# Kernel tuning notes

Measured on AMD Instinct MI355X. Metric: run time of the kernel, lower is better.

The kernel has to match this reference:

```python
import jax, jax.numpy as jnp
import numpy as np

N, M, D, H, T = 8192, 8192, 64, 32, 8
KERNEL_SCALE = 1.0


def setup_inputs() -> dict:
    key = jax.random.key(0)
    ks = jax.random.split(key, 8)
    s1 = 1.0 / np.sqrt(D)
    s2 = 1.0 / np.sqrt(H)
    return {
        "X": jax.random.normal(ks[0], (N, D), jnp.float32),
        "Y": jax.random.normal(ks[1], (M, D), jnp.float32),
        "Y_target": jax.random.normal(ks[2], (M, T), jnp.float32),
        "W1": jax.random.normal(ks[3], (D, H), jnp.float32) * s1,
        "b1": jnp.zeros((H,), jnp.float32),
        "W2": jax.random.normal(ks[4], (H, H), jnp.float32) * s2,
        "b2": jnp.zeros((H,), jnp.float32),
        "W3": jax.random.normal(ks[5], (H, H), jnp.float32) * s2,
        "b3": jnp.zeros((H,), jnp.float32),
    }


def _mlp(x, W1, b1, W2, b2, W3, b3):
    h = jax.nn.relu(x @ W1 + b1)
    h = jax.nn.relu(h @ W2 + b2)
    return jax.nn.relu(h @ W3 + b3)


def reference(X, Y, Y_target, W1, b1, W2, b2, W3, b3):
    Xf = _mlp(X, W1, b1, W2, b2, W3, b3)  # [N, H]
    Yf = _mlp(Y, W1, b1, W2, b2, W3, b3)  # [M, H]
    sq = (
        jnp.sum(Xf * Xf, axis=1, keepdims=True)
        + jnp.sum(Yf * Yf, axis=1)[None, :]
        - 2.0 * (Xf @ Yf.T)
    )
    sq = jnp.maximum(sq, 0.0)  # guard tiny negatives from cancellation
    kernel = jnp.exp(-sq / (2.0 * KERNEL_SCALE**2))  # [N, M]
    weights = kernel / jnp.sum(kernel, axis=1, keepdims=True)
    return weights @ Y_target  # [N, T]
```

## Files before the change

kernel.cpp:

```cpp
#include <hip/hip_runtime.h>
#include <hip/hip_bf16.h>
#include <cstddef>

#define N_ROWS 8192
#define M_ROWS 8192
#define D_IN   64
#define H_DIM  32
#define T_OUT  8
#define FDIM   48

#define NSPLIT   32
#define JSLICE   (M_ROWS / NSPLIT)
#define JTILE    32
#define NTILES   (JSLICE / JTILE)
#define LOG2E    1.4426950408889634f
#define NHALF_SC (-0.72134752044448169f)

typedef _Float16 half8  __attribute__((ext_vector_type(8)));
typedef _Float16 half4v __attribute__((ext_vector_type(4)));
typedef __fp16   fp16x2 __attribute__((ext_vector_type(2)));
typedef float    f32x16 __attribute__((ext_vector_type(16)));

__device__ __forceinline__ half8 ld_h8(const _Float16* p) {
    return *(const half8*)p;
}

__global__ __launch_bounds__(256) void feat_kernel(
    const float* __restrict__ X, const float* __restrict__ Y,
    const float* __restrict__ W1, const float* __restrict__ b1,
    const float* __restrict__ W2, const float* __restrict__ b2,
    const float* __restrict__ W3, const float* __restrict__ b3,
    _Float16* __restrict__ fh, _Float16* __restrict__ fl)
{
    __shared__ float xs [32 * 65];
    __shared__ float w1l[64 * 36];
    __shared__ float w2l[32 * 36];
    __shared__ float w3l[32 * 36];
    __shared__ float h1t[32 * 33];
    __shared__ float h2t[32 * 33];
    __shared__ float psums[8 * 32];
    __shared__ float bl[96];

    const int tid = threadIdx.x;
    const int rowbase = blockIdx.x * 32;
    const bool isX = rowbase < N_ROWS;
    const float* src = isX ? (X + (size_t)rowbase * D_IN)
                           : (Y + (size_t)(rowbase - N_ROWS) * D_IN);

    {
        const float4* g4 = (const float4*)src;
        int i0 = tid * 2;
        float4 v0 = g4[i0], v1 = g4[i0 + 1];
        int f0 = tid * 8;
        int r = f0 >> 6, c = f0 & 63;
        float* dst = xs + r * 65 + c;
        dst[0] = v0.x; dst[1] = v0.y; dst[2] = v0.z; dst[3] = v0.w;
        dst[4] = v1.x; dst[5] = v1.y; dst[6] = v1.z; dst[7] = v1.w;
    }
    {
        const float4* g4 = (const float4*)W1;
        int i0 = tid * 2;
        float4 v0 = g4[i0], v1 = g4[i0 + 1];
        int f0 = tid * 8;
        int r = f0 >> 5, c = f0 & 31;
        float* dst = w1l + r * 36 + c;
        ((float4*)dst)[0] = v0; ((float4*)dst)[1] = v1;
    }
    {
        int f0 = tid * 4;
        int r = f0 >> 5, c = f0 & 31;
        *(float4*)(w2l + r * 36 + c) = ((const float4*)W2)[tid];
        *(float4*)(w3l + r * 36 + c) = ((const float4*)W3)[tid];
    }
    if (tid < 32) { bl[tid] = b1[tid]; bl[32 + tid] = b2[tid]; bl[64 + tid] = b3[tid]; }
    __syncthreads();

    const int r  = tid & 31;
    const int c0 = (tid >> 5) * 4;

    float4 a1 = *(const float4*)(bl + c0);
    #pragma unroll
    for (int k = 0; k < 64; ++k) {
        float xv = xs[r * 65 + k];
        float4 w = *(const float4*)(w1l + k * 36 + c0);
        a1.x = fmaf(xv, w.x, a1.x);
        a1.y = fmaf(xv, w.y, a1.y);
        a1.z = fmaf(xv, w.z, a1.z);
        a1.w = fmaf(xv, w.w, a1.w);
    }
    h1t[(c0 + 0) * 33 + r] = fmaxf(a1.x, 0.f);
    h1t[(c0 + 1) * 33 + r] = fmaxf(a1.y, 0.f);
    h1t[(c0 + 2) * 33 + r] = fmaxf(a1.z, 0.f);
    h1t[(c0 + 3) * 33 + r] = fmaxf(a1.w, 0.f);
    __syncthreads();

    float4 a2 = *(const float4*)(bl + 32 + c0);
    #pragma unroll
    for (int k = 0; k < 32; ++k) {
        float xv = h1t[k * 33 + r];
        float4 w = *(const float4*)(w2l + k * 36 + c0);
        a2.x = fmaf(xv, w.x, a2.x);
        a2.y = fmaf(xv, w.y, a2.y);
        a2.z = fmaf(xv, w.z, a2.z);
        a2.w = fmaf(xv, w.w, a2.w);
    }
    h2t[(c0 + 0) * 33 + r] = fmaxf(a2.x, 0.f);
    h2t[(c0 + 1) * 33 + r] = fmaxf(a2.y, 0.f);
    h2t[(c0 + 2) * 33 + r] = fmaxf(a2.z, 0.f);
    h2t[(c0 + 3) * 33 + r] = fmaxf(a2.w, 0.f);
    __syncthreads();

    float4 a3 = *(const float4*)(bl + 64 + c0);
    #pragma unroll
    for (int k = 0; k < 32; ++k) {
        float xv = h2t[k * 33 + r];
        float4 w = *(const float4*)(w3l + k * 36 + c0);
        a3.x = fmaf(xv, w.x, a3.x);
        a3.y = fmaf(xv, w.y, a3.y);
        a3.z = fmaf(xv, w.z, a3.z);
        a3.w = fmaf(xv, w.w, a3.w);
    }
    float v0 = fmaxf(a3.x, 0.f), v1 = fmaxf(a3.y, 0.f);
    float v2 = fmaxf(a3.z, 0.f), v3 = fmaxf(a3.w, 0.f);

    psums[(tid >> 5) * 32 + r] = v0 * v0 + v1 * v1 + v2 * v2 + v3 * v3;

    const float scale = isX ? LOG2E : 1.0f;
    union { _Float16 h[4]; uint2 u; } hh, ll;
    float sv0 = v0 * scale, sv1 = v1 * scale, sv2 = v2 * scale, sv3 = v3 * scale;
    hh.h[0] = (_Float16)sv0; hh.h[1] = (_Float16)sv1;
    hh.h[2] = (_Float16)sv2; hh.h[3] = (_Float16)sv3;
    ll.h[0] = (_Float16)(sv0 - (float)hh.h[0]);
    ll.h[1] = (_Float16)(sv1 - (float)hh.h[1]);
    ll.h[2] = (_Float16)(sv2 - (float)hh.h[2]);
    ll.h[3] = (_Float16)(sv3 - (float)hh.h[3]);
    const size_t fo = (size_t)(rowbase + r) * FDIM + c0;
    *(uint2*)(fh + fo) = hh.u;
    *(uint2*)(fl + fo) = ll.u;

    __syncthreads();
    if (tid < 32) {
        float nrm = 0.f;
        #pragma unroll
        for (int g = 0; g < 8; ++g) nrm += psums[g * 32 + tid];
        float qn = NHALF_SC * nrm;
        float d32 = isX ? qn : 1.0f;
        float d33 = isX ? 1.0f : qn;
        union { _Float16 h[16]; uint4 q[2]; } eh, el;
        #pragma unroll
        for (int i = 0; i < 16; ++i) { eh.h[i] = (_Float16)0.f; el.h[i] = (_Float16)0.f; }
        _Float16 h32 = (_Float16)d32, h33 = (_Float16)d33;
        eh.h[0] = h32; eh.h[1] = h33;
        el.h[0] = (_Float16)(d32 - (float)h32);
        el.h[1] = (_Float16)(d33 - (float)h33);
        const size_t eo = (size_t)(rowbase + tid) * FDIM + 32;
        *(uint4*)(fh + eo) = eh.q[0]; *(uint4*)(fh + eo + 8) = eh.q[1];
        *(uint4*)(fl + eo) = el.q[0]; *(uint4*)(fl + eo + 8) = el.q[1];
    }
}

__global__ __launch_bounds__(256) void ytt_kernel(
    const float* __restrict__ Yt,
    _Float16* __restrict__ yfh, _Float16* __restrict__ yfl)
{
    const int idx = blockIdx.x * 256 + threadIdx.x;
    const int lane = idx & 63;
    const int jtg  = idx >> 6;
    const int g    = jtg & 3;
    const int jt   = jtg >> 2;
    const int t    = lane & 31;
    const int h    = lane >> 5;
    const int j    = jt * 32 + g * 8 + h * 4;
    union { _Float16 hh[4]; uint2 u; } H, L;
    #pragma unroll
    for (int i = 0; i < 4; ++i) {
        float v = (t < T_OUT) ? Yt[(size_t)(j + i) * T_OUT + t]
                              : (t == 8 ? 1.0f : 0.0f);
        _Float16 hi = (_Float16)v;
        H.hh[i] = hi;
        L.hh[i] = (_Float16)(v - (float)hi);
    }
    *(uint2*)(yfh + (size_t)idx * 4) = H.u;
    *(uint2*)(yfl + (size_t)idx * 4) = L.u;
}

__global__ __launch_bounds__(256, 4) void pair_kernel(
    const _Float16* __restrict__ fh, const _Float16* __restrict__ fl,
    const _Float16* __restrict__ yfh, const _Float16* __restrict__ yfl,
    float* __restrict__ pout, float* __restrict__ psum)
{
    const int tid  = threadIdx.x;
    const int wave = tid >> 6;
    const int lane = tid & 63;
    const int n    = lane & 31;
    const int h    = lane >> 5;

    const int rowbase = blockIdx.x * 128 + wave * 32;
    const int s       = blockIdx.y;
    const int jstart  = s * JSLICE;

    const _Float16* qb  = fh + (size_t)(rowbase + n) * FDIM + h * 8;
    const _Float16* qbl = fl + (size_t)(rowbase + n) * FDIM + h * 8;
    half8 qh0 = ld_h8(qb);        half8 qh1 = ld_h8(qb + 16);
    half8 qh2 = ld_h8(qb + 32);
    half8 ql0 = ld_h8(qbl);       half8 ql1 = ld_h8(qbl + 16);
    half8 ql2 = ld_h8(qbl + 32);

    f32x16 o = {};

    for (int jt = 0; jt < NTILES; ++jt) {
        const int jbase = jstart + jt * JTILE;

        const _Float16* ka  = fh + (size_t)(N_ROWS + jbase + n) * FDIM + h * 8;
        const _Float16* kal = fl + (size_t)(N_ROWS + jbase + n) * FDIM + h * 8;
        half8 kh0 = ld_h8(ka);        half8 kh1 = ld_h8(ka + 16);
        half8 kh2 = ld_h8(ka + 32);
        half8 kl0 = ld_h8(kal);       half8 kl1 = ld_h8(kal + 16);
        half8 kl2 = ld_h8(kal + 32);

        f32x16 acc = {};
        acc = __builtin_amdgcn_mfma_f32_32x32x16_f16(kh0, qh0, acc, 0, 0, 0);
        acc = __builtin_amdgcn_mfma_f32_32x32x16_f16(kh1, qh1, acc, 0, 0, 0);
        acc = __builtin_amdgcn_mfma_f32_32x32x16_f16(kh2, qh2, acc, 0, 0, 0);
        acc = __builtin_amdgcn_mfma_f32_32x32x16_f16(kh0, ql0, acc, 0, 0, 0);
        acc = __builtin_amdgcn_mfma_f32_32x32x16_f16(kh1, ql1, acc, 0, 0, 0);
        acc = __builtin_amdgcn_mfma_f32_32x32x16_f16(kh2, ql2, acc, 0, 0, 0);
        acc = __builtin_amdgcn_mfma_f32_32x32x16_f16(kl0, qh0, acc, 0, 0, 0);
        acc = __builtin_amdgcn_mfma_f32_32x32x16_f16(kl1, qh1, acc, 0, 0, 0);
        acc = __builtin_amdgcn_mfma_f32_32x32x16_f16(kl2, qh2, acc, 0, 0, 0);

        half4v phi[4], plo[4];
        #pragma unroll
        for (int g = 0; g < 4; ++g) {
            float w0 = __builtin_amdgcn_exp2f(fminf(acc[4*g+0], 0.f));
            float w1 = __builtin_amdgcn_exp2f(fminf(acc[4*g+1], 0.f));
            float w2 = __builtin_amdgcn_exp2f(fminf(acc[4*g+2], 0.f));
            float w3 = __builtin_amdgcn_exp2f(fminf(acc[4*g+3], 0.f));
            fp16x2 p01 = __builtin_amdgcn_cvt_pkrtz(w0, w1);
            fp16x2 p23 = __builtin_amdgcn_cvt_pkrtz(w2, w3);
            fp16x2 l01 = __builtin_amdgcn_cvt_pkrtz(w0 - (float)p01[0],
                                                    w1 - (float)p01[1]);
            fp16x2 l23 = __builtin_amdgcn_cvt_pkrtz(w2 - (float)p23[0],
                                                    w3 - (float)p23[1]);
            union { unsigned int u[2]; half4v v; } ph, pl;
            ph.u[0] = __builtin_bit_cast(unsigned int, p01);
            ph.u[1] = __builtin_bit_cast(unsigned int, p23);
            pl.u[0] = __builtin_bit_cast(unsigned int, l01);
            pl.u[1] = __builtin_bit_cast(unsigned int, l23);
            phi[g] = ph.v; plo[g] = pl.v;
        }

        const size_t yb = ((size_t)(((size_t)jstart / JTILE + jt) * 4) * 64 + lane) * 4;
        #pragma unroll
        for (int g = 0; g < 4; ++g) {
            half4v bh = *(const half4v*)(yfh + yb + (size_t)g * 256);
            half4v bl = *(const half4v*)(yfl + yb + (size_t)g * 256);
            o = __builtin_amdgcn_mfma_f32_32x32x8f16(phi[g], bh, o, 0, 0, 0);
            o = __builtin_amdgcn_mfma_f32_32x32x8f16(plo[g], bh, o, 0, 0, 0);
            o = __builtin_amdgcn_mfma_f32_32x32x8f16(phi[g], bl, o, 0, 0, 0);
        }
    }

    const int t = n;
    if (t <= 8) {
        #pragma unroll
        for (int r = 0; r < 16; ++r) {
            int i = (r & 3) + 8 * (r >> 2) + 4 * h;
            int row = rowbase + i;
            float v = o[r];
            if (t < 8)
                pout[((size_t)s * N_ROWS + row) * T_OUT + t] = v;
            else
                psum[(size_t)s * N_ROWS + row] = v;
        }
    }
}

__global__ __launch_bounds__(256) void reduce_kernel(
    const float* __restrict__ pout, const float* __restrict__ psum,
    float* __restrict__ out)
{
    const int id = blockIdx.x * 256 + threadIdx.x;
    const int i = id >> 3;
    float sv = 0.f, sw = 0.f;
    #pragma unroll
    for (int s = 0; s < NSPLIT; ++s) {
        sv += pout[(size_t)s * N_ROWS * T_OUT + id];
        sw += psum[(size_t)s * N_ROWS + i];
    }
    out[id] = sv / sw;
}

extern "C" void kernel_launch(void* const* d_in, const int* in_sizes, int n_in,
                              void* d_out, int out_size, void* d_ws, size_t ws_size,
                              hipStream_t stream)
{
    const float* X  = (const float*)d_in[0];
    const float* Y  = (const float*)d_in[1];
    const float* Yt = (const float*)d_in[2];
    const float* W1 = (const float*)d_in[3];
    const float* b1 = (const float*)d_in[4];
    const float* W2 = (const float*)d_in[5];
    const float* b2 = (const float*)d_in[6];
    const float* W3 = (const float*)d_in[7];
    const float* b3 = (const float*)d_in[8];
    float* out = (float*)d_out;

    char* ws = (char*)d_ws;
    const size_t n_feat = (size_t)(N_ROWS + M_ROWS) * FDIM;
    _Float16* fh  = (_Float16*)ws;   ws += n_feat * 2;
    _Float16* fl  = (_Float16*)ws;   ws += n_feat * 2;
    const size_t n_yf = (size_t)(M_ROWS / JTILE) * 4 * 64 * 4;
    _Float16* yfh = (_Float16*)ws;   ws += n_yf * 2;
    _Float16* yfl = (_Float16*)ws;   ws += n_yf * 2;
    float*    pout = (float*)ws;     ws += (size_t)NSPLIT * N_ROWS * T_OUT * 4;
    float*    psum = (float*)ws;

    feat_kernel<<<(N_ROWS + M_ROWS) / 32, 256, 0, stream>>>(
        X, Y, W1, b1, W2, b2, W3, b3, fh, fl);
    ytt_kernel<<<(M_ROWS / JTILE) * 4 * 64 / 256, 256, 0, stream>>>(Yt, yfh, yfl);

    dim3 grid2(N_ROWS / 128, NSPLIT);
    pair_kernel<<<grid2, 256, 0, stream>>>(fh, fl, yfh, yfl, pout, psum);

    reduce_kernel<<<(N_ROWS * T_OUT) / 256, 256, 0, stream>>>(pout, psum, out);
}
```

Measured before the change: 125.7 us.

## Store features in MFMA-fragment tiled layout and drop low-part weight MFMA

The feature kernel now writes features in a per-32-row tile layout that matches the MFMA operand fragments, so each lane's 16-byte loads in the pair kernel are contiguous across the wave instead of strided by row. Separately, the pair kernel drops the low half of the fp16 split for the softmax weights, removing one MFMA per group along with the residual conversions. This lowers the precision of the weighted sum, since the weights now carry only fp16 accuracy.

```diff
diff --git a/kernel.cpp b/kernel.cpp
--- a/kernel.cpp
+++ b/kernel.cpp
@@ -24,6 +24,7 @@
 __device__ __forceinline__ half8 ld_h8(const _Float16* p) {
     return *(const half8*)p;
 }
+
 
 __global__ __launch_bounds__(256) void feat_kernel(
     const float* __restrict__ X, const float* __restrict__ Y,
@@ -134,9 +135,13 @@
     ll.h[1] = (_Float16)(sv1 - (float)hh.h[1]);
     ll.h[2] = (_Float16)(sv2 - (float)hh.h[2]);
     ll.h[3] = (_Float16)(sv3 - (float)hh.h[3]);
-    const size_t fo = (size_t)(rowbase + r) * FDIM + c0;
-    *(uint2*)(fh + fo) = hh.u;
-    *(uint2*)(fl + fo) = ll.u;
+    {
+        const int tile = blockIdx.x;
+        const int ch = c0 >> 4, hb = (c0 >> 3) & 1, off = c0 & 7;
+        const size_t fi = (((size_t)(tile * 3 + ch) * 64) + hb * 32 + r) * 8 + off;
+        *(uint2*)(fh + fi) = hh.u;
+        *(uint2*)(fl + fi) = ll.u;
+    }
 
     __syncthreads();
     if (tid < 32) {
@@ -146,16 +151,18 @@
         float qn = NHALF_SC * nrm;
         float d32 = isX ? qn : 1.0f;
         float d33 = isX ? 1.0f : qn;
-        union { _Float16 h[16]; uint4 q[2]; } eh, el;
-        #pragma unroll
-        for (int i = 0; i < 16; ++i) { eh.h[i] = (_Float16)0.f; el.h[i] = (_Float16)0.f; }
+        union { _Float16 h[8]; uint4 q; } eh, el, ez;
+        #pragma unroll
+        for (int i = 0; i < 8; ++i) { eh.h[i] = (_Float16)0.f; el.h[i] = (_Float16)0.f; ez.h[i] = (_Float16)0.f; }
         _Float16 h32 = (_Float16)d32, h33 = (_Float16)d33;
         eh.h[0] = h32; eh.h[1] = h33;
         el.h[0] = (_Float16)(d32 - (float)h32);
         el.h[1] = (_Float16)(d33 - (float)h33);
-        const size_t eo = (size_t)(rowbase + tid) * FDIM + 32;
-        *(uint4*)(fh + eo) = eh.q[0]; *(uint4*)(fh + eo + 8) = eh.q[1];
-        *(uint4*)(fl + eo) = el.q[0]; *(uint4*)(fl + eo + 8) = el.q[1];
+        const int tile = blockIdx.x;
+        const size_t f0 = (((size_t)(tile * 3 + 2) * 64) + tid) * 8;
+        const size_t f1 = (((size_t)(tile * 3 + 2) * 64) + 32 + tid) * 8;
+        *(uint4*)(fh + f0) = eh.q;  *(uint4*)(fh + f1) = ez.q;
+        *(uint4*)(fl + f0) = el.q;  *(uint4*)(fl + f1) = ez.q;
     }
 }
 
@@ -195,28 +202,30 @@
     const int n    = lane & 31;
     const int h    = lane >> 5;
 
-    const int rowbase = blockIdx.x * 128 + wave * 32;
+    const int rowtile = blockIdx.x * 4 + wave;
+    const int rowbase = rowtile * 32;
     const int s       = blockIdx.y;
-    const int jstart  = s * JSLICE;
-
-    const _Float16* qb  = fh + (size_t)(rowbase + n) * FDIM + h * 8;
-    const _Float16* qbl = fl + (size_t)(rowbase + n) * FDIM + h * 8;
-    half8 qh0 = ld_h8(qb);        half8 qh1 = ld_h8(qb + 16);
-    half8 qh2 = ld_h8(qb + 32);
-    half8 ql0 = ld_h8(qbl);       half8 ql1 = ld_h8(qbl + 16);
-    half8 ql2 = ld_h8(qbl + 32);
+
+    const size_t qoff = ((size_t)rowtile * 3) * 512 + (size_t)lane * 8;
+    half8 qh0 = ld_h8(fh + qoff);
+    half8 qh1 = ld_h8(fh + qoff + 512);
+    half8 qh2 = ld_h8(fh + qoff + 1024);
+    half8 ql0 = ld_h8(fl + qoff);
+    half8 ql1 = ld_h8(fl + qoff + 512);
+    half8 ql2 = ld_h8(fl + qoff + 1024);
 
     f32x16 o = {};
 
+    const int ktile0 = (N_ROWS / 32) + s * NTILES;
+
     for (int jt = 0; jt < NTILES; ++jt) {
-        const int jbase = jstart + jt * JTILE;
-
-        const _Float16* ka  = fh + (size_t)(N_ROWS + jbase + n) * FDIM + h * 8;
-        const _Float16* kal = fl + (size_t)(N_ROWS + jbase + n) * FDIM + h * 8;
-        half8 kh0 = ld_h8(ka);        half8 kh1 = ld_h8(ka + 16);
-        half8 kh2 = ld_h8(ka + 32);
-        half8 kl0 = ld_h8(kal);       half8 kl1 = ld_h8(kal + 16);
-        half8 kl2 = ld_h8(kal + 32);
+        const size_t koff = ((size_t)(ktile0 + jt) * 3) * 512 + (size_t)lane * 8;
+        half8 kh0 = ld_h8(fh + koff);
+        half8 kh1 = ld_h8(fh + koff + 512);
+        half8 kh2 = ld_h8(fh + koff + 1024);
+        half8 kl0 = ld_h8(fl + koff);
+        half8 kl1 = ld_h8(fl + koff + 512);
+        half8 kl2 = ld_h8(fl + koff + 1024);
 
         f32x16 acc = {};
         acc = __builtin_amdgcn_mfma_f32_32x32x16_f16(kh0, qh0, acc, 0, 0, 0);
@@ -229,7 +238,7 @@
         acc = __builtin_amdgcn_mfma_f32_32x32x16_f16(kl1, qh1, acc, 0, 0, 0);
         acc = __builtin_amdgcn_mfma_f32_32x32x16_f16(kl2, qh2, acc, 0, 0, 0);
 
-        half4v phi[4], plo[4];
+        half4v phi[4];
         #pragma unroll
         for (int g = 0; g < 4; ++g) {
             float w0 = __builtin_amdgcn_exp2f(fminf(acc[4*g+0], 0.f));
@@ -238,26 +247,19 @@
             float w3 = __builtin_amdgcn_exp2f(fminf(acc[4*g+3], 0.f));
             fp16x2 p01 = __builtin_amdgcn_cvt_pkrtz(w0, w1);
             fp16x2 p23 = __builtin_amdgcn_cvt_pkrtz(w2, w3);
-            fp16x2 l01 = __builtin_amdgcn_cvt_pkrtz(w0 - (float)p01[0],
-                                                    w1 - (float)p01[1]);
-            fp16x2 l23 = __builtin_amdgcn_cvt_pkrtz(w2 - (float)p23[0],
-                                                    w3 - (float)p23[1]);
-            union { unsigned int u[2]; half4v v; } ph, pl;
+            union { unsigned int u[2]; half4v v; } ph;
             ph.u[0] = __builtin_bit_cast(unsigned int, p01);
             ph.u[1] = __builtin_bit_cast(unsigned int, p23);
-            pl.u[0] = __builtin_bit_cast(unsigned int, l01);
-            pl.u[1] = __builtin_bit_cast(unsigned int, l23);
-            phi[g] = ph.v; plo[g] = pl.v;
+            phi[g] = ph.v;
         }
 
-        const size_t yb = ((size_t)(((size_t)jstart / JTILE + jt) * 4) * 64 + lane) * 4;
+        const size_t yb = ((size_t)((s * NTILES + jt) * 4) * 64 + lane) * 4;
         #pragma unroll
         for (int g = 0; g < 4; ++g) {
             half4v bh = *(const half4v*)(yfh + yb + (size_t)g * 256);
-            half4v bl = *(const half4v*)(yfl + yb + (size_t)g * 256);
+            half4v bv = *(const half4v*)(yfl + yb + (size_t)g * 256);
             o = __builtin_amdgcn_mfma_f32_32x32x8f16(phi[g], bh, o, 0, 0, 0);
-            o = __builtin_amdgcn_mfma_f32_32x32x8f16(plo[g], bh, o, 0, 0, 0);
-            o = __builtin_amdgcn_mfma_f32_32x32x8f16(phi[g], bl, o, 0, 0, 0);
+            o = __builtin_amdgcn_mfma_f32_32x32x8f16(phi[g], bv, o, 0, 0, 0);
         }
     }
 
@@ -307,7 +309,7 @@
     float* out = (float*)d_out;
 
     char* ws = (char*)d_ws;
-    const size_t n_feat = (size_t)(N_ROWS + M_ROWS) * FDIM;
+    const size_t n_feat = (size_t)((N_ROWS + M_ROWS) / 32) * 3 * 512;
     _Float16* fh  = (_Float16*)ws;   ws += n_feat * 2;
     _Float16* fl  = (_Float16*)ws;   ws += n_feat * 2;
     const size_t n_yf = (size_t)(M_ROWS / JTILE) * 4 * 64 * 4;
```

New measurement: 121.2 us. -3.6%, faster.
